# Performance work log

Measured on AMD Instinct MI355X. Metric: run time of the kernel, lower is better.

The kernel has to match this reference:

```python
import jax, jax.numpy as jnp
import numpy as np

B, N = 2, 2000
C_IN, RH, RW = 256, 7, 7
D_FLAT = C_IN * RH * RW  # 12544
D_OUT = 1024
NUM_CLASSES = 10


def setup_inputs() -> dict:
    key = jax.random.key(0)
    ks = jax.random.split(key, 10)
    s1 = 1.0 / np.sqrt(D_FLAT)
    s2 = 1.0 / np.sqrt(D_OUT)
    return {
        "features": jax.random.normal(ks[0], (B, N, C_IN, RH, RW), jnp.float32),
        "boxes": jax.random.normal(ks[1], (B, N, 5), jnp.float32),
        "w1": jax.random.uniform(ks[2], (D_FLAT, D_OUT), jnp.float32, -s1, s1),
        "b1": jax.random.uniform(ks[3], (D_OUT,), jnp.float32, -s1, s1),
        "w2": jax.random.uniform(ks[4], (D_OUT, D_OUT), jnp.float32, -s2, s2),
        "b2": jax.random.uniform(ks[5], (D_OUT,), jnp.float32, -s2, s2),
        "wc": jax.random.uniform(ks[6], (D_OUT, NUM_CLASSES + 1), jnp.float32, -s2, s2),
        "bc": jax.random.uniform(ks[7], (NUM_CLASSES + 1,), jnp.float32, -s2, s2),
        "wr": jax.random.uniform(ks[8], (D_OUT, 5), jnp.float32, -s2, s2),
        "br": jax.random.uniform(ks[9], (5,), jnp.float32, -s2, s2),
    }


def reference(features, boxes, w1, b1, w2, b2, wc, bc, wr, br):
    # Flatten(start_dim=2): [B, N, C*7*7]
    x = features.reshape(B, N, D_FLAT)
    # fc: Linear -> ReLU -> Linear -> ReLU
    h = jax.nn.relu(jnp.einsum("bnd,de->bne", x, w1) + b1)
    h = jax.nn.relu(jnp.einsum("bnd,de->bne", h, w2) + b2)
    classification = jnp.einsum("bnd,dc->bnc", h, wc) + bc  # [B, N, num_classes+1]
    regression = jnp.einsum("bnd,dr->bnr", h, wr) + br      # [B, N, 5]
    boxes_out = boxes + regression
    rois = boxes
    return classification, boxes_out, rois
```

## Files before the change

### kernel.cpp

```cpp
#include <hip/hip_runtime.h>
#include <stdint.h>

#define GAS __attribute__((address_space(1)))
#define LAS __attribute__((address_space(3)))

typedef short bf16x8 __attribute__((ext_vector_type(8)));
typedef float f32x4 __attribute__((ext_vector_type(4)));
typedef unsigned short u16x8 __attribute__((ext_vector_type(8)));

__device__ __forceinline__ unsigned short f2bf(float f) {
  union { float f; uint32_t u; } v; v.f = f;
  uint32_t r = v.u + 0x7FFFu + ((v.u >> 16) & 1u);
  return (unsigned short)(r >> 16);
}

__global__ __launch_bounds__(256) void cvt_kernel(const float* __restrict__ src,
                                                  unsigned short* __restrict__ dst,
                                                  long n8) {
  long i = (long)blockIdx.x * blockDim.x + threadIdx.x;
  if (i >= n8) return;
  const float4* s4 = (const float4*)src;
  float4 a = s4[i * 2];
  float4 b = s4[i * 2 + 1];
  u16x8 o;
  o[0] = f2bf(a.x); o[1] = f2bf(a.y); o[2] = f2bf(a.z); o[3] = f2bf(a.w);
  o[4] = f2bf(b.x); o[5] = f2bf(b.y); o[6] = f2bf(b.z); o[7] = f2bf(b.w);
  ((u16x8*)dst)[i] = o;
}

__global__ __launch_bounds__(256) void transpose_cvt(const float* __restrict__ src,
                                                     unsigned short* __restrict__ dst,
                                                     int R, int C) {
  __shared__ unsigned short tile[32][33];
  int tx = threadIdx.x, ty = threadIdx.y;
  int r0 = blockIdx.y * 32, c0 = blockIdx.x * 32;
#pragma unroll
  for (int i = 0; i < 32; i += 8)
    tile[ty + i][tx] = f2bf(src[(long)(r0 + ty + i) * C + c0 + tx]);
  __syncthreads();
#pragma unroll
  for (int i = 0; i < 32; i += 8)
    dst[(long)(c0 + ty + i) * R + r0 + tx] = tile[tx][ty + i];
}

__global__ __launch_bounds__(256) void bias_relu_cvt(const float* __restrict__ acc,
                                                     const float* __restrict__ bias,
                                                     unsigned short* __restrict__ dst) {
  long i = (long)blockIdx.x * 256 + threadIdx.x;
  const float4* a4 = (const float4*)acc;
  float4 a = a4[i * 2];
  float4 b = a4[i * 2 + 1];
  int col = (int)((i * 8) & 1023);
  const float4* b4 = (const float4*)(bias + col);
  float4 ba = b4[0], bb = b4[1];
  u16x8 o;
  o[0] = f2bf(fmaxf(a.x + ba.x, 0.f)); o[1] = f2bf(fmaxf(a.y + ba.y, 0.f));
  o[2] = f2bf(fmaxf(a.z + ba.z, 0.f)); o[3] = f2bf(fmaxf(a.w + ba.w, 0.f));
  o[4] = f2bf(fmaxf(b.x + bb.x, 0.f)); o[5] = f2bf(fmaxf(b.y + bb.y, 0.f));
  o[6] = f2bf(fmaxf(b.z + bb.z, 0.f)); o[7] = f2bf(fmaxf(b.w + bb.w, 0.f));
  ((u16x8*)dst)[i] = o;
}

__global__ __launch_bounds__(512, 2) void gemm1_8w(const unsigned short* __restrict__ A,
                                                   const unsigned short* __restrict__ Bt,
                                                   float* __restrict__ Cv, int M, int K,
                                                   int kIters) {
  __shared__ unsigned short lds[65536];
  const int tid = threadIdx.x;
  const int lane = tid & 63;
  const int wave = tid >> 6;
  const int wm = wave >> 2;
  const int wn = wave & 3;

  const int b = blockIdx.x;
  const int xcd = b & 7;
  const int slot = b >> 3;
  const int panel = xcd + 8 * (slot >> 4);
  const int bz = panel >> 2;
  const int bx = panel & 3;
  const int by = slot & 15;

  const long rowBase = (long)by * 256;
  const long colBase = (long)bx * 256;
  const int kStart = bz * kIters * 64;

  f32x4 acc[8][4];
#pragma unroll
  for (int i = 0; i < 8; i++)
#pragma unroll
    for (int j = 0; j < 4; j++) acc[i][j] = (f32x4){0.f, 0.f, 0.f, 0.f};

  long g8[8];
  int ldsOff8[8];
#pragma unroll
  for (int i = 0; i < 8; ++i) {
    int flat = i * 512 + tid;
    int s = flat & 2047;
    int r = s >> 3;
    int q = s & 7;
    int kq = ((q ^ (r & 7)) * 8) + kStart;
    long row;
    if (flat >= 2048) {
      row = colBase + r;
    } else {
      row = rowBase + r;
      if (row >= M) row = M - 1;
    }
    g8[i] = row * (long)K + kq;
    ldsOff8[i] = flat * 8;
  }

#pragma unroll
  for (int i = 0; i < 8; ++i) {
    const unsigned short* src = (i < 4) ? A : Bt;
    __builtin_amdgcn_global_load_lds((const GAS void*)(src + g8[i]),
                                     (LAS void*)(lds + ldsOff8[i]), 16, 0, 0);
  }
  asm volatile("s_waitcnt vmcnt(0)" ::: "memory");
  __builtin_amdgcn_s_barrier();
  asm volatile("" ::: "memory");

  const int l15 = lane & 15;
  const int lxor = lane & 7;
  const int chi = lane >> 4;

  for (int t = 0; t < kIters; ++t) {
    const int cb = (t & 1) << 15;
    const int nb = cb ^ 32768;
    const long kc = (long)(t + 1) * 64;
    const bool doStage = (t + 1 < kIters);

#pragma unroll
    for (int p = 0; p < 4; ++p) {
      const int qi = p >> 1;
      const int qj = p & 1;
      bf16x8 af[4][2], bf[2][2];
#pragma unroll
      for (int ks = 0; ks < 2; ++ks) {
        const int slotk = (((ks * 4 + chi) ^ lxor) << 3);
#pragma unroll
        for (int i = 0; i < 4; ++i) {
          const int mr = wm * 128 + qi * 64 + i * 16 + l15;
          af[i][ks] = *(const bf16x8*)(lds + cb + mr * 64 + slotk);
        }
#pragma unroll
        for (int j = 0; j < 2; ++j) {
          const int nr = wn * 64 + qj * 32 + j * 16 + l15;
          bf[j][ks] = *(const bf16x8*)(lds + cb + 16384 + nr * 64 + slotk);
        }
      }
      if (doStage && p < 2) {
#pragma unroll
        for (int l = 0; l < 4; ++l) {
          const int idx = p * 4 + l;
          const unsigned short* src = (idx < 4) ? A : Bt;
          __builtin_amdgcn_global_load_lds((const GAS void*)(src + g8[idx] + kc),
                                           (LAS void*)(lds + nb + ldsOff8[idx]), 16, 0, 0);
        }
      }
      __builtin_amdgcn_s_barrier();
      asm volatile("s_waitcnt lgkmcnt(0)" ::: "memory");
      __builtin_amdgcn_sched_barrier(0);
      __builtin_amdgcn_s_setprio(1);
#pragma unroll
      for (int i = 0; i < 4; ++i)
#pragma unroll
        for (int j = 0; j < 2; ++j) {
          acc[qi * 4 + i][qj * 2 + j] = __builtin_amdgcn_mfma_f32_16x16x32_bf16(
              af[i][0], bf[j][0], acc[qi * 4 + i][qj * 2 + j], 0, 0, 0);
          acc[qi * 4 + i][qj * 2 + j] = __builtin_amdgcn_mfma_f32_16x16x32_bf16(
              af[i][1], bf[j][1], acc[qi * 4 + i][qj * 2 + j], 0, 0, 0);
        }
      __builtin_amdgcn_s_setprio(0);
      if (p == 3) {
        asm volatile("s_waitcnt vmcnt(0)" ::: "memory");
      }
      __builtin_amdgcn_s_barrier();
    }
    asm volatile("" ::: "memory");
  }

  const int cq = lane & 15;
  const int rq = (lane >> 4) << 2;
#pragma unroll
  for (int i = 0; i < 8; ++i) {
#pragma unroll
    for (int j = 0; j < 4; ++j) {
      const int col = (int)colBase + wn * 64 + j * 16 + cq;
#pragma unroll
      for (int r = 0; r < 4; ++r) {
        long grow = rowBase + wm * 128 + i * 16 + rq + r;
        if (grow < M) unsafeAtomicAdd(&Cv[grow * 1024 + col], acc[i][j][r]);
      }
    }
  }
}

__global__ __launch_bounds__(256, 2) void gemm2_direct(const unsigned short* __restrict__ A,
                                                       const unsigned short* __restrict__ Bt,
                                                       const float* __restrict__ bias,
                                                       float* __restrict__ Cv, int M) {
  const int K = 1024;
  __shared__ unsigned short lA[128 * 64];
  __shared__ unsigned short lB[64 * 64];
  const int tid = threadIdx.x;
  const int lane = tid & 63;
  const int wave = tid >> 6;
  const int wm = wave >> 1, wn = wave & 1;

  const int b = blockIdx.x;
  const int xcd = b & 7;
  const int slot = b >> 3;
  const int bx = slot & 15;
  const int by = xcd * 4 + (slot >> 4);

  const long rowBase = (long)by * 128;
  const long colBase = (long)bx * 64;

  f32x4 acc[4][2];
#pragma unroll
  for (int i = 0; i < 4; i++)
#pragma unroll
    for (int j = 0; j < 2; j++) acc[i][j] = (f32x4){0.f, 0.f, 0.f, 0.f};

  long gA[4], gB[2];
#pragma unroll
  for (int it = 0; it < 4; ++it) {
    int f = it * 256 + tid;
    int r = f >> 3;
    int q = f & 7;
    int kq = (q ^ (r & 7)) * 8;
    long ar = rowBase + r;
    if (ar >= M) ar = M - 1;
    gA[it] = ar * (long)K + kq;
  }
#pragma unroll
  for (int it = 0; it < 2; ++it) {
    int f = it * 256 + tid;
    int r = f >> 3;
    int q = f & 7;
    int kq = (q ^ (r & 7)) * 8;
    gB[it] = ((long)(colBase + r)) * K + kq;
  }

  for (int ki = 0; ki < 16; ++ki) {
    const long kc = (long)ki * 64;
#pragma unroll
    for (int it = 0; it < 4; ++it) {
      int f = it * 256 + tid;
      __builtin_amdgcn_global_load_lds((const GAS void*)(A + gA[it] + kc),
                                       (LAS void*)(lA + f * 8), 16, 0, 0);
    }
#pragma unroll
    for (int it = 0; it < 2; ++it) {
      int f = it * 256 + tid;
      __builtin_amdgcn_global_load_lds((const GAS void*)(Bt + gB[it] + kc),
                                       (LAS void*)(lB + f * 8), 16, 0, 0);
    }
    __syncthreads();
#pragma unroll
    for (int ks = 0; ks < 64; ks += 32) {
      bf16x8 af[4], bf[2];
      const int c = (ks >> 3) + (lane >> 4);
      const int slotk = (c ^ (lane & 7)) << 3;
      const int mr = wm * 64 + (lane & 15);
      const int nr = wn * 32 + (lane & 15);
#pragma unroll
      for (int i = 0; i < 4; i++)
        af[i] = *(const bf16x8*)(lA + (mr + i * 16) * 64 + slotk);
#pragma unroll
      for (int j = 0; j < 2; j++)
        bf[j] = *(const bf16x8*)(lB + (nr + j * 16) * 64 + slotk);
#pragma unroll
      for (int i = 0; i < 4; i++)
#pragma unroll
        for (int j = 0; j < 2; j++)
          acc[i][j] = __builtin_amdgcn_mfma_f32_16x16x32_bf16(af[i], bf[j], acc[i][j], 0, 0, 0);
    }
    __syncthreads();
  }

  const int cq = lane & 15;
  const int rq = (lane >> 4) * 4;
#pragma unroll
  for (int i = 0; i < 4; i++) {
#pragma unroll
    for (int j = 0; j < 2; j++) {
      int col = (int)colBase + wn * 32 + j * 16 + cq;
      float bv = bias[col];
#pragma unroll
      for (int r = 0; r < 4; r++) {
        long grow = rowBase + wm * 64 + i * 16 + rq + r;
        if (grow < M) {
          float v = acc[i][j][r] + bv;
          Cv[grow * 1024 + col] = v > 0.f ? v : 0.f;
        }
      }
    }
  }
}

__global__ __launch_bounds__(256) void head_kernel(
    const float* __restrict__ H2, const float* __restrict__ wc, const float* __restrict__ bc,
    const float* __restrict__ wr, const float* __restrict__ br, const float* __restrict__ boxes,
    float* __restrict__ cls, float* __restrict__ bout, float* __restrict__ rois) {
  const int lane = threadIdx.x & 63;
  const int wave = threadIdx.x >> 6;
  const int row = blockIdx.x * 4 + wave;
  const float* h = H2 + (long)row * 1024;
  float acc[16];
#pragma unroll
  for (int c = 0; c < 16; c++) acc[c] = 0.f;
#pragma unroll
  for (int i = 0; i < 16; i++) {
    int d = i * 64 + lane;
    float hv = h[d];
#pragma unroll
    for (int c = 0; c < 11; c++) acc[c] += hv * wc[d * 11 + c];
#pragma unroll
    for (int c = 0; c < 5; c++) acc[11 + c] += hv * wr[d * 5 + c];
  }
#pragma unroll
  for (int off = 32; off >= 1; off >>= 1) {
#pragma unroll
    for (int c = 0; c < 16; c++) acc[c] += __shfl_down(acc[c], off);
  }
  if (lane == 0) {
#pragma unroll
    for (int c = 0; c < 11; c++) cls[row * 11 + c] = acc[c] + bc[c];
#pragma unroll
    for (int c = 0; c < 5; c++) {
      float rg = acc[11 + c] + br[c];
      float bx = boxes[row * 5 + c];
      bout[row * 5 + c] = bx + rg;
      rois[row * 5 + c] = bx;
    }
  }
}

extern "C" void kernel_launch(void* const* d_in, const int* in_sizes, int n_in,
                              void* d_out, int out_size, void* d_ws, size_t ws_size,
                              hipStream_t stream) {
  const float* features = (const float*)d_in[0];
  const float* boxes = (const float*)d_in[1];
  const float* w1 = (const float*)d_in[2];
  const float* b1 = (const float*)d_in[3];
  const float* w2 = (const float*)d_in[4];
  const float* b2 = (const float*)d_in[5];
  const float* wc = (const float*)d_in[6];
  const float* bc = (const float*)d_in[7];
  const float* wr = (const float*)d_in[8];
  const float* br = (const float*)d_in[9];

  char* ws = (char*)d_ws;
  unsigned short* Xb  = (unsigned short*)ws;
  unsigned short* W1T = (unsigned short*)(ws + 100352000);
  unsigned short* W2T = (unsigned short*)(ws + 126042112);
  unsigned short* H1  = (unsigned short*)(ws + 128139264);
  float*          H1f = (float*)(ws + 136331264);
  float*          H2  = (float*)(ws + 152715264);

  hipMemsetAsync(H1f, 0, 16384000, stream);
  cvt_kernel<<<24500, 256, 0, stream>>>(features, Xb, 6272000);
  transpose_cvt<<<dim3(32, 392), dim3(32, 8), 0, stream>>>(w1, W1T, 12544, 1024);
  transpose_cvt<<<dim3(32, 32), dim3(32, 8), 0, stream>>>(w2, W2T, 1024, 1024);
  gemm1_8w<<<256, 512, 0, stream>>>(Xb, W1T, H1f, 4000, 12544, 49);
  bias_relu_cvt<<<2000, 256, 0, stream>>>(H1f, b1, H1);
  gemm2_direct<<<512, 256, 0, stream>>>(H1, W2T, b2, H2, 4000);
  float* cls = (float*)d_out;
  float* bout = cls + 44000;
  float* rois = cls + 64000;
  head_kernel<<<1000, 256, 0, stream>>>(H2, wc, bc, wr, br, boxes, cls, bout, rois);
}
```

Measured before the change: 532.2 us.

## Retile GEMM1 to 256x128 blocks with triple-buffered LDS prefetch pipeline

Replaces the 256x256 double-buffered GEMM1 kernel with a 256x128 tile, 4x2 wave layout, and a three-stage LDS ring buffer that prefetches two K-steps ahead. Waiting on vmcnt lets global-to-LDS loads overlap with MFMA work, with one barrier pair per K-step instead of per quarter. Grid doubles to 512 blocks and the split-K mapping is reworked. The cost is more LDS (144KB per block) and lower per-wave arithmetic intensity, which increases A-matrix reloads.

```diff
diff --git a/kernel.cpp b/kernel.cpp
--- a/kernel.cpp
+++ b/kernel.cpp
@@ -61,135 +61,140 @@
   ((u16x8*)dst)[i] = o;
 }
 
-__global__ __launch_bounds__(512, 2) void gemm1_8w(const unsigned short* __restrict__ A,
-                                                   const unsigned short* __restrict__ Bt,
-                                                   float* __restrict__ Cv, int M, int K,
-                                                   int kIters) {
-  __shared__ unsigned short lds[65536];
+__global__ __launch_bounds__(512, 2) void gemm1_pipe(const unsigned short* __restrict__ A,
+                                                     const unsigned short* __restrict__ Bt,
+                                                     float* __restrict__ Cv, int M, int K,
+                                                     int kIters) {
+  __shared__ unsigned short lds[73728];
   const int tid = threadIdx.x;
   const int lane = tid & 63;
   const int wave = tid >> 6;
-  const int wm = wave >> 2;
-  const int wn = wave & 3;
+  const int wm = wave >> 1;
+  const int wn = wave & 1;
 
   const int b = blockIdx.x;
   const int xcd = b & 7;
   const int slot = b >> 3;
-  const int panel = xcd + 8 * (slot >> 4);
-  const int bz = panel >> 2;
-  const int bx = panel & 3;
-  const int by = slot & 15;
+  const int bx = slot & 7;
+  const int pair = slot >> 3;
+  const int bz = xcd >> 1;
+  const int by = (xcd & 1) * 8 + pair;
 
   const long rowBase = (long)by * 256;
-  const long colBase = (long)bx * 256;
+  const long colBase = (long)bx * 128;
   const int kStart = bz * kIters * 64;
 
-  f32x4 acc[8][4];
-#pragma unroll
-  for (int i = 0; i < 8; i++)
+  f32x4 acc[4][4];
+#pragma unroll
+  for (int i = 0; i < 4; i++)
 #pragma unroll
     for (int j = 0; j < 4; j++) acc[i][j] = (f32x4){0.f, 0.f, 0.f, 0.f};
 
-  long g8[8];
-  int ldsOff8[8];
-#pragma unroll
-  for (int i = 0; i < 8; ++i) {
+  long g6[6];
+  int lo6[6];
+#pragma unroll
+  for (int i = 0; i < 6; ++i) {
     int flat = i * 512 + tid;
-    int s = flat & 2047;
+    int s = (flat < 2048) ? flat : (flat - 2048);
     int r = s >> 3;
     int q = s & 7;
     int kq = ((q ^ (r & 7)) * 8) + kStart;
     long row;
-    if (flat >= 2048) {
-      row = colBase + r;
-    } else {
+    if (flat < 2048) {
       row = rowBase + r;
       if (row >= M) row = M - 1;
-    }
-    g8[i] = row * (long)K + kq;
-    ldsOff8[i] = flat * 8;
-  }
-
-#pragma unroll
-  for (int i = 0; i < 8; ++i) {
+    } else {
+      row = colBase + r;
+    }
+    g6[i] = row * (long)K + kq;
+    lo6[i] = flat * 8;
+  }
+
+#pragma unroll
+  for (int i = 0; i < 6; ++i) {
     const unsigned short* src = (i < 4) ? A : Bt;
-    __builtin_amdgcn_global_load_lds((const GAS void*)(src + g8[i]),
-                                     (LAS void*)(lds + ldsOff8[i]), 16, 0, 0);
-  }
-  asm volatile("s_waitcnt vmcnt(0)" ::: "memory");
-  __builtin_amdgcn_s_barrier();
-  asm volatile("" ::: "memory");
+    __builtin_amdgcn_global_load_lds((const GAS void*)(src + g6[i]),
+                                     (LAS void*)(lds + lo6[i]), 16, 0, 0);
+  }
+#pragma unroll
+  for (int i = 0; i < 6; ++i) {
+    const unsigned short* src = (i < 4) ? A : Bt;
+    __builtin_amdgcn_global_load_lds((const GAS void*)(src + g6[i] + 64),
+                                     (LAS void*)(lds + 24576 + lo6[i]), 16, 0, 0);
+  }
 
   const int l15 = lane & 15;
   const int lxor = lane & 7;
   const int chi = lane >> 4;
 
+  int cbuf = 0;
+  int nbuf = 2;
+
   for (int t = 0; t < kIters; ++t) {
-    const int cb = (t & 1) << 15;
-    const int nb = cb ^ 32768;
-    const long kc = (long)(t + 1) * 64;
-    const bool doStage = (t + 1 < kIters);
-
-#pragma unroll
-    for (int p = 0; p < 4; ++p) {
-      const int qi = p >> 1;
-      const int qj = p & 1;
-      bf16x8 af[4][2], bf[2][2];
-#pragma unroll
-      for (int ks = 0; ks < 2; ++ks) {
-        const int slotk = (((ks * 4 + chi) ^ lxor) << 3);
-#pragma unroll
-        for (int i = 0; i < 4; ++i) {
-          const int mr = wm * 128 + qi * 64 + i * 16 + l15;
-          af[i][ks] = *(const bf16x8*)(lds + cb + mr * 64 + slotk);
-        }
-#pragma unroll
-        for (int j = 0; j < 2; ++j) {
-          const int nr = wn * 64 + qj * 32 + j * 16 + l15;
-          bf[j][ks] = *(const bf16x8*)(lds + cb + 16384 + nr * 64 + slotk);
-        }
-      }
-      if (doStage && p < 2) {
-#pragma unroll
-        for (int l = 0; l < 4; ++l) {
-          const int idx = p * 4 + l;
-          const unsigned short* src = (idx < 4) ? A : Bt;
-          __builtin_amdgcn_global_load_lds((const GAS void*)(src + g8[idx] + kc),
-                                           (LAS void*)(lds + nb + ldsOff8[idx]), 16, 0, 0);
-        }
-      }
-      __builtin_amdgcn_s_barrier();
-      asm volatile("s_waitcnt lgkmcnt(0)" ::: "memory");
-      __builtin_amdgcn_sched_barrier(0);
-      __builtin_amdgcn_s_setprio(1);
-#pragma unroll
-      for (int i = 0; i < 4; ++i)
-#pragma unroll
-        for (int j = 0; j < 2; ++j) {
-          acc[qi * 4 + i][qj * 2 + j] = __builtin_amdgcn_mfma_f32_16x16x32_bf16(
-              af[i][0], bf[j][0], acc[qi * 4 + i][qj * 2 + j], 0, 0, 0);
-          acc[qi * 4 + i][qj * 2 + j] = __builtin_amdgcn_mfma_f32_16x16x32_bf16(
-              af[i][1], bf[j][1], acc[qi * 4 + i][qj * 2 + j], 0, 0, 0);
-        }
-      __builtin_amdgcn_s_setprio(0);
-      if (p == 3) {
-        asm volatile("s_waitcnt vmcnt(0)" ::: "memory");
-      }
-      __builtin_amdgcn_s_barrier();
-    }
     asm volatile("" ::: "memory");
+    __builtin_amdgcn_s_barrier();
+    asm volatile("" ::: "memory");
+    if (t + 2 < kIters) {
+      const long kc = (long)(t + 2) * 64;
+      const int nbase = nbuf * 24576;
+#pragma unroll
+      for (int i = 0; i < 6; ++i) {
+        const unsigned short* src = (i < 4) ? A : Bt;
+        __builtin_amdgcn_global_load_lds((const GAS void*)(src + g6[i] + kc),
+                                         (LAS void*)(lds + nbase + lo6[i]), 16, 0, 0);
+      }
+    }
+    if (t < kIters - 2) {
+      asm volatile("s_waitcnt vmcnt(12)" ::: "memory");
+    } else if (t == kIters - 2) {
+      asm volatile("s_waitcnt vmcnt(6)" ::: "memory");
+    } else {
+      asm volatile("s_waitcnt vmcnt(0)" ::: "memory");
+    }
+    __builtin_amdgcn_s_barrier();
+    asm volatile("" ::: "memory");
+    __builtin_amdgcn_sched_barrier(0);
+
+    const int cb = cbuf * 24576;
+    bf16x8 af[4][2], bfr[4][2];
+#pragma unroll
+    for (int ks = 0; ks < 2; ++ks) {
+      const int slotk = (((ks * 4) + chi) ^ lxor) << 3;
+#pragma unroll
+      for (int i = 0; i < 4; ++i) {
+        const int mr = wm * 64 + i * 16 + l15;
+        af[i][ks] = *(const bf16x8*)(lds + cb + mr * 64 + slotk);
+      }
+#pragma unroll
+      for (int j = 0; j < 4; ++j) {
+        const int nr = wn * 64 + j * 16 + l15;
+        bfr[j][ks] = *(const bf16x8*)(lds + cb + 16384 + nr * 64 + slotk);
+      }
+    }
+    __builtin_amdgcn_s_setprio(1);
+#pragma unroll
+    for (int i = 0; i < 4; ++i)
+#pragma unroll
+      for (int j = 0; j < 4; ++j) {
+        acc[i][j] = __builtin_amdgcn_mfma_f32_16x16x32_bf16(af[i][0], bfr[j][0], acc[i][j], 0, 0, 0);
+        acc[i][j] = __builtin_amdgcn_mfma_f32_16x16x32_bf16(af[i][1], bfr[j][1], acc[i][j], 0, 0, 0);
+      }
+    __builtin_amdgcn_s_setprio(0);
+
+    cbuf = (cbuf == 2) ? 0 : cbuf + 1;
+    nbuf = (nbuf == 2) ? 0 : nbuf + 1;
   }
 
   const int cq = lane & 15;
   const int rq = (lane >> 4) << 2;
 #pragma unroll
-  for (int i = 0; i < 8; ++i) {
+  for (int i = 0; i < 4; ++i) {
 #pragma unroll
     for (int j = 0; j < 4; ++j) {
       const int col = (int)colBase + wn * 64 + j * 16 + cq;
 #pragma unroll
       for (int r = 0; r < 4; ++r) {
-        long grow = rowBase + wm * 128 + i * 16 + rq + r;
+        long grow = rowBase + wm * 64 + i * 16 + rq + r;
         if (grow < M) unsafeAtomicAdd(&Cv[grow * 1024 + col], acc[i][j][r]);
       }
     }
@@ -364,7 +369,7 @@
   cvt_kernel<<<24500, 256, 0, stream>>>(features, Xb, 6272000);
   transpose_cvt<<<dim3(32, 392), dim3(32, 8), 0, stream>>>(w1, W1T, 12544, 1024);
   transpose_cvt<<<dim3(32, 32), dim3(32, 8), 0, stream>>>(w2, W2T, 1024, 1024);
-  gemm1_8w<<<256, 512, 0, stream>>>(Xb, W1T, H1f, 4000, 12544, 49);
+  gemm1_pipe<<<512, 512, 0, stream>>>(Xb, W1T, H1f, 4000, 12544, 49);
   bias_relu_cvt<<<2000, 256, 0, stream>>>(H1f, b1, H1);
   gemm2_direct<<<512, 256, 0, stream>>>(H1, W2T, b2, H2, 4000);
   float* cls = (float*)d_out;
```

After: 532.8 us. Within noise of the previous version (+0.1%).

## Fuse fp32 feature conversion and bias-ReLU epilogue into non-split-K GEMM1

Applied to the files above, without the earlier changes.

GEMM1 now reads fp32 features straight from global memory, converts them to bf16 in registers with v_cvt_pk_bf16_f32 and stores them to LDS. This removes the separate conversion pass and the bf16 copy of the features. Split-K with atomics is replaced by full-K 128x64 tiles, so bias+ReLU+bf16 conversion happens in the epilogue and the memset and bias_relu kernel are dropped. The two weight transposes are merged into one launch. The trade-off is smaller tiles with less data reuse, twice the A-operand bytes read per tile, and a long serial K loop per block (196 iterations) with register prefetch instead of async LDS loads.

```diff
diff --git a/kernel.cpp b/kernel.cpp
--- a/kernel.cpp
+++ b/kernel.cpp
@@ -14,26 +14,28 @@
   return (unsigned short)(r >> 16);
 }
 
-__global__ __launch_bounds__(256) void cvt_kernel(const float* __restrict__ src,
-                                                  unsigned short* __restrict__ dst,
-                                                  long n8) {
-  long i = (long)blockIdx.x * blockDim.x + threadIdx.x;
-  if (i >= n8) return;
-  const float4* s4 = (const float4*)src;
-  float4 a = s4[i * 2];
-  float4 b = s4[i * 2 + 1];
-  u16x8 o;
-  o[0] = f2bf(a.x); o[1] = f2bf(a.y); o[2] = f2bf(a.z); o[3] = f2bf(a.w);
-  o[4] = f2bf(b.x); o[5] = f2bf(b.y); o[6] = f2bf(b.z); o[7] = f2bf(b.w);
-  ((u16x8*)dst)[i] = o;
-}
-
-__global__ __launch_bounds__(256) void transpose_cvt(const float* __restrict__ src,
-                                                     unsigned short* __restrict__ dst,
-                                                     int R, int C) {
+__device__ __forceinline__ uint32_t cvtpk(float lo, float hi) {
+  uint32_t r;
+  asm("v_cvt_pk_bf16_f32 %0, %1, %2" : "=v"(r) : "v"(lo), "v"(hi));
+  return r;
+}
+
+__global__ __launch_bounds__(256) void prep_transpose(const float* __restrict__ w1,
+                                                      const float* __restrict__ w2,
+                                                      unsigned short* __restrict__ W1T,
+                                                      unsigned short* __restrict__ W2T) {
   __shared__ unsigned short tile[32][33];
   int tx = threadIdx.x, ty = threadIdx.y;
-  int r0 = blockIdx.y * 32, c0 = blockIdx.x * 32;
+  const float* src;
+  unsigned short* dst;
+  int R, yb;
+  if ((int)blockIdx.y < 392) {
+    src = w1; dst = W1T; R = 12544; yb = blockIdx.y;
+  } else {
+    src = w2; dst = W2T; R = 1024; yb = blockIdx.y - 392;
+  }
+  const int C = 1024;
+  int r0 = yb * 32, c0 = blockIdx.x * 32;
 #pragma unroll
   for (int i = 0; i < 32; i += 8)
     tile[ty + i][tx] = f2bf(src[(long)(r0 + ty + i) * C + c0 + tx]);
@@ -43,154 +45,173 @@
     dst[(long)(c0 + ty + i) * R + r0 + tx] = tile[tx][ty + i];
 }
 
-__global__ __launch_bounds__(256) void bias_relu_cvt(const float* __restrict__ acc,
-                                                     const float* __restrict__ bias,
-                                                     unsigned short* __restrict__ dst) {
-  long i = (long)blockIdx.x * 256 + threadIdx.x;
-  const float4* a4 = (const float4*)acc;
-  float4 a = a4[i * 2];
-  float4 b = a4[i * 2 + 1];
-  int col = (int)((i * 8) & 1023);
-  const float4* b4 = (const float4*)(bias + col);
-  float4 ba = b4[0], bb = b4[1];
-  u16x8 o;
-  o[0] = f2bf(fmaxf(a.x + ba.x, 0.f)); o[1] = f2bf(fmaxf(a.y + ba.y, 0.f));
-  o[2] = f2bf(fmaxf(a.z + ba.z, 0.f)); o[3] = f2bf(fmaxf(a.w + ba.w, 0.f));
-  o[4] = f2bf(fmaxf(b.x + bb.x, 0.f)); o[5] = f2bf(fmaxf(b.y + bb.y, 0.f));
-  o[6] = f2bf(fmaxf(b.z + bb.z, 0.f)); o[7] = f2bf(fmaxf(b.w + bb.w, 0.f));
-  ((u16x8*)dst)[i] = o;
-}
-
-__global__ __launch_bounds__(512, 2) void gemm1_8w(const unsigned short* __restrict__ A,
-                                                   const unsigned short* __restrict__ Bt,
-                                                   float* __restrict__ Cv, int M, int K,
-                                                   int kIters) {
-  __shared__ unsigned short lds[65536];
+__global__ __launch_bounds__(256, 2) void gemm1_fused(const float* __restrict__ A,
+                                                      const unsigned short* __restrict__ Bt,
+                                                      const float* __restrict__ bias,
+                                                      unsigned short* __restrict__ H1,
+                                                      int M, int K, int kIters) {
+  __shared__ unsigned short lA[2 * 8192];
+  __shared__ unsigned short lB[2 * 4096];
   const int tid = threadIdx.x;
   const int lane = tid & 63;
   const int wave = tid >> 6;
-  const int wm = wave >> 2;
-  const int wn = wave & 3;
+  const int wm = wave >> 1, wn = wave & 1;
 
   const int b = blockIdx.x;
   const int xcd = b & 7;
   const int slot = b >> 3;
-  const int panel = xcd + 8 * (slot >> 4);
-  const int bz = panel >> 2;
-  const int bx = panel & 3;
-  const int by = slot & 15;
-
-  const long rowBase = (long)by * 256;
-  const long colBase = (long)bx * 256;
-  const int kStart = bz * kIters * 64;
-
-  f32x4 acc[8][4];
-#pragma unroll
-  for (int i = 0; i < 8; i++)
-#pragma unroll
-    for (int j = 0; j < 4; j++) acc[i][j] = (f32x4){0.f, 0.f, 0.f, 0.f};
-
-  long g8[8];
-  int ldsOff8[8];
-#pragma unroll
-  for (int i = 0; i < 8; ++i) {
-    int flat = i * 512 + tid;
-    int s = flat & 2047;
+  const int bx = slot & 15;
+  const int by = xcd * 4 + (slot >> 4);
+
+  const int rowBase = by * 128;
+  const int colBase = bx * 64;
+
+  f32x4 acc[4][2];
+#pragma unroll
+  for (int i = 0; i < 4; i++)
+#pragma unroll
+    for (int j = 0; j < 2; j++) acc[i][j] = (f32x4){0.f, 0.f, 0.f, 0.f};
+
+  int gA[4], aLds[4];
+#pragma unroll
+  for (int i = 0; i < 4; ++i) {
+    int s = i * 256 + tid;
     int r = s >> 3;
     int q = s & 7;
-    int kq = ((q ^ (r & 7)) * 8) + kStart;
-    long row;
-    if (flat >= 2048) {
-      row = colBase + r;
-    } else {
-      row = rowBase + r;
-      if (row >= M) row = M - 1;
-    }
-    g8[i] = row * (long)K + kq;
-    ldsOff8[i] = flat * 8;
-  }
-
-#pragma unroll
-  for (int i = 0; i < 8; ++i) {
-    const unsigned short* src = (i < 4) ? A : Bt;
-    __builtin_amdgcn_global_load_lds((const GAS void*)(src + g8[i]),
-                                     (LAS void*)(lds + ldsOff8[i]), 16, 0, 0);
+    int kq = (q ^ (r & 7)) * 8;
+    int ar = rowBase + r;
+    if (ar >= M) ar = M - 1;
+    gA[i] = ar * K + kq;
+    aLds[i] = s * 8;
+  }
+  int gB[2], bLds[2];
+#pragma unroll
+  for (int i = 0; i < 2; ++i) {
+    int s = i * 256 + tid;
+    int r = s >> 3;
+    int q = s & 7;
+    int kq = (q ^ (r & 7)) * 8;
+    gB[i] = (colBase + r) * K + kq;
+    bLds[i] = s * 8;
+  }
+
+  float4 pre[4][2];
+
+#pragma unroll
+  for (int i = 0; i < 2; ++i)
+    __builtin_amdgcn_global_load_lds((const GAS void*)(Bt + gB[i]),
+                                     (LAS void*)(lB + bLds[i]), 16, 0, 0);
+#pragma unroll
+  for (int i = 0; i < 4; ++i) {
+    const float4* p = (const float4*)(A + gA[i]);
+    pre[i][0] = p[0];
+    pre[i][1] = p[1];
+  }
+#pragma unroll
+  for (int i = 0; i < 4; ++i) {
+    uint4 v;
+    v.x = cvtpk(pre[i][0].x, pre[i][0].y);
+    v.y = cvtpk(pre[i][0].z, pre[i][0].w);
+    v.z = cvtpk(pre[i][1].x, pre[i][1].y);
+    v.w = cvtpk(pre[i][1].z, pre[i][1].w);
+    *(uint4*)(lA + aLds[i]) = v;
   }
   asm volatile("s_waitcnt vmcnt(0)" ::: "memory");
+  asm volatile("s_waitcnt lgkmcnt(0)" ::: "memory");
   __builtin_amdgcn_s_barrier();
   asm volatile("" ::: "memory");
+#pragma unroll
+  for (int i = 0; i < 4; ++i) {
+    const float4* p = (const float4*)(A + gA[i] + 64);
+    pre[i][0] = p[0];
+    pre[i][1] = p[1];
+  }
 
   const int l15 = lane & 15;
   const int lxor = lane & 7;
   const int chi = lane >> 4;
 
   for (int t = 0; t < kIters; ++t) {
-    const int cb = (t & 1) << 15;
-    const int nb = cb ^ 32768;
-    const long kc = (long)(t + 1) * 64;
-    const bool doStage = (t + 1 < kIters);
-
-#pragma unroll
-    for (int p = 0; p < 4; ++p) {
-      const int qi = p >> 1;
-      const int qj = p & 1;
-      bf16x8 af[4][2], bf[2][2];
-#pragma unroll
-      for (int ks = 0; ks < 2; ++ks) {
-        const int slotk = (((ks * 4 + chi) ^ lxor) << 3);
+    const int cur = t & 1;
+    const int nxt = cur ^ 1;
+    const int cA = cur * 8192, nA = nxt * 8192;
+    const int cB = cur * 4096, nB = nxt * 4096;
+    const bool more = (t + 1 < kIters);
+
+    if (more) {
+      const int kc = (t + 1) * 64;
+#pragma unroll
+      for (int i = 0; i < 2; ++i)
+        __builtin_amdgcn_global_load_lds((const GAS void*)(Bt + gB[i] + kc),
+                                         (LAS void*)(lB + nB + bLds[i]), 16, 0, 0);
+    }
+
+    bf16x8 af[4][2], bf[2][2];
+#pragma unroll
+    for (int ks = 0; ks < 2; ++ks) {
+      const int slotk = (((ks * 4) + chi) ^ lxor) << 3;
+#pragma unroll
+      for (int i = 0; i < 4; ++i) {
+        const int mr = wm * 64 + i * 16 + l15;
+        af[i][ks] = *(const bf16x8*)(lA + cA + mr * 64 + slotk);
+      }
+#pragma unroll
+      for (int j = 0; j < 2; ++j) {
+        const int nr = wn * 32 + j * 16 + l15;
+        bf[j][ks] = *(const bf16x8*)(lB + cB + nr * 64 + slotk);
+      }
+    }
+    __builtin_amdgcn_s_setprio(1);
+#pragma unroll
+    for (int i = 0; i < 4; ++i)
+#pragma unroll
+      for (int j = 0; j < 2; ++j) {
+        acc[i][j] = __builtin_amdgcn_mfma_f32_16x16x32_bf16(af[i][0], bf[j][0], acc[i][j], 0, 0, 0);
+        acc[i][j] = __builtin_amdgcn_mfma_f32_16x16x32_bf16(af[i][1], bf[j][1], acc[i][j], 0, 0, 0);
+      }
+    __builtin_amdgcn_s_setprio(0);
+
+    if (more) {
+      asm volatile("s_waitcnt vmcnt(0)" ::: "memory");
+#pragma unroll
+      for (int i = 0; i < 4; ++i) {
+        uint4 v;
+        v.x = cvtpk(pre[i][0].x, pre[i][0].y);
+        v.y = cvtpk(pre[i][0].z, pre[i][0].w);
+        v.z = cvtpk(pre[i][1].x, pre[i][1].y);
+        v.w = cvtpk(pre[i][1].z, pre[i][1].w);
+        *(uint4*)(lA + nA + aLds[i]) = v;
+      }
+      if (t + 2 < kIters) {
+        const int kc2 = (t + 2) * 64;
 #pragma unroll
         for (int i = 0; i < 4; ++i) {
-          const int mr = wm * 128 + qi * 64 + i * 16 + l15;
-          af[i][ks] = *(const bf16x8*)(lds + cb + mr * 64 + slotk);
+          const float4* p = (const float4*)(A + gA[i] + kc2);
+          pre[i][0] = p[0];
+          pre[i][1] = p[1];
         }
-#pragma unroll
-        for (int j = 0; j < 2; ++j) {
-          const int nr = wn * 64 + qj * 32 + j * 16 + l15;
-          bf[j][ks] = *(const bf16x8*)(lds + cb + 16384 + nr * 64 + slotk);
-        }
-      }
-      if (doStage && p < 2) {
-#pragma unroll
-        for (int l = 0; l < 4; ++l) {
-          const int idx = p * 4 + l;
-          const unsigned short* src = (idx < 4) ? A : Bt;
-          __builtin_amdgcn_global_load_lds((const GAS void*)(src + g8[idx] + kc),
-                                           (LAS void*)(lds + nb + ldsOff8[idx]), 16, 0, 0);
-        }
-      }
-      __builtin_amdgcn_s_barrier();
+      }
       asm volatile("s_waitcnt lgkmcnt(0)" ::: "memory");
-      __builtin_amdgcn_sched_barrier(0);
-      __builtin_amdgcn_s_setprio(1);
-#pragma unroll
-      for (int i = 0; i < 4; ++i)
-#pragma unroll
-        for (int j = 0; j < 2; ++j) {
-          acc[qi * 4 + i][qj * 2 + j] = __builtin_amdgcn_mfma_f32_16x16x32_bf16(
-              af[i][0], bf[j][0], acc[qi * 4 + i][qj * 2 + j], 0, 0, 0);
-          acc[qi * 4 + i][qj * 2 + j] = __builtin_amdgcn_mfma_f32_16x16x32_bf16(
-              af[i][1], bf[j][1], acc[qi * 4 + i][qj * 2 + j], 0, 0, 0);
-        }
-      __builtin_amdgcn_s_setprio(0);
-      if (p == 3) {
-        asm volatile("s_waitcnt vmcnt(0)" ::: "memory");
-      }
-      __builtin_amdgcn_s_barrier();
-    }
+    }
+    __builtin_amdgcn_s_barrier();
     asm volatile("" ::: "memory");
   }
 
   const int cq = lane & 15;
   const int rq = (lane >> 4) << 2;
 #pragma unroll
-  for (int i = 0; i < 8; ++i) {
-#pragma unroll
-    for (int j = 0; j < 4; ++j) {
-      const int col = (int)colBase + wn * 64 + j * 16 + cq;
+  for (int i = 0; i < 4; ++i) {
+#pragma unroll
+    for (int j = 0; j < 2; ++j) {
+      const int col = colBase + wn * 32 + j * 16 + cq;
+      const float bv = bias[col];
 #pragma unroll
       for (int r = 0; r < 4; ++r) {
-        long grow = rowBase + wm * 128 + i * 16 + rq + r;
-        if (grow < M) unsafeAtomicAdd(&Cv[grow * 1024 + col], acc[i][j][r]);
+        int grow = rowBase + wm * 64 + i * 16 + rq + r;
+        if (grow < M) {
+          float v = acc[i][j][r] + bv;
+          H1[(long)grow * 1024 + col] = f2bf(v > 0.f ? v : 0.f);
+        }
       }
     }
   }
@@ -353,19 +374,13 @@
   const float* br = (const float*)d_in[9];
 
   char* ws = (char*)d_ws;
-  unsigned short* Xb  = (unsigned short*)ws;
-  unsigned short* W1T = (unsigned short*)(ws + 100352000);
-  unsigned short* W2T = (unsigned short*)(ws + 126042112);
-  unsigned short* H1  = (unsigned short*)(ws + 128139264);
-  float*          H1f = (float*)(ws + 136331264);
-  float*          H2  = (float*)(ws + 152715264);
-
-  hipMemsetAsync(H1f, 0, 16384000, stream);
-  cvt_kernel<<<24500, 256, 0, stream>>>(features, Xb, 6272000);
-  transpose_cvt<<<dim3(32, 392), dim3(32, 8), 0, stream>>>(w1, W1T, 12544, 1024);
-  transpose_cvt<<<dim3(32, 32), dim3(32, 8), 0, stream>>>(w2, W2T, 1024, 1024);
-  gemm1_8w<<<256, 512, 0, stream>>>(Xb, W1T, H1f, 4000, 12544, 49);
-  bias_relu_cvt<<<2000, 256, 0, stream>>>(H1f, b1, H1);
+  unsigned short* W1T = (unsigned short*)ws;
+  unsigned short* W2T = (unsigned short*)(ws + 25690112);
+  unsigned short* H1  = (unsigned short*)(ws + 27787264);
+  float*          H2  = (float*)(ws + 35979264);
+
+  prep_transpose<<<dim3(32, 424), dim3(32, 8), 0, stream>>>(w1, w2, W1T, W2T);
+  gemm1_fused<<<512, 256, 0, stream>>>(features, W1T, b1, H1, 4000, 12544, 196);
   gemm2_direct<<<512, 256, 0, stream>>>(H1, W2T, b2, H2, 4000);
   float* cls = (float*)d_out;
   float* bout = cls + 44000;
```

Result: slower. 582.6 us (+9.5%).
